# Kernel tuning notes

Measured on AMD Instinct MI355X. Metric: run time of the kernel, lower is better.

Reference implementation:

```python
import jax, jax.numpy as jnp
import numpy as np

N, FR, P, B = 8192, 128, 4194304, 64
LH1, LH2 = 128, 64

def _mlp(x, W1, b1, W2, b2, W3, b3):
    h = jnp.tanh(x @ W1 + b1)
    h = jnp.tanh(h @ W2 + b2)
    return h @ W3 + b3  # [N, 1]

def setup_inputs() -> dict:
    key = jax.random.key(0)
    ks = jax.random.split(key, 12)
    r = jax.random.normal(ks[0], (N, FR), jnp.float32)
    xyz = jax.random.uniform(ks[1], (N, 3), jnp.float32) * 60.0  # box so distances >> sigma
    p0 = jax.random.randint(ks[2], (P,), 0, N)
    off = jax.random.randint(ks[3], (P,), 1, N)  # avoid self-pairs (D2=0)
    pairs = jnp.stack([p0, (p0 + off) % N], axis=1).astype(jnp.int32)
    num_pairs = jnp.full((B,), P // B, dtype=jnp.int32)
    def lin(k, fin, fout):
        return (jax.random.normal(k, (fin, fout), jnp.float32) / np.sqrt(fin)).astype(jnp.float32)
    sW1, sW2, sW3 = lin(ks[4], FR, LH1), lin(ks[5], LH1, LH2), lin(ks[6], LH2, 1)
    eW1, eW2, eW3 = lin(ks[7], FR, LH1), lin(ks[8], LH1, LH2), lin(ks[9], LH2, 1)
    z1, z2, z3 = jnp.zeros((LH1,), jnp.float32), jnp.zeros((LH2,), jnp.float32), jnp.zeros((1,), jnp.float32)
    return dict(r=r, xyz=xyz, pairs=pairs, num_pairs=num_pairs,
                sW1=sW1, sb1=z1, sW2=sW2, sb2=z2, sW3=sW3, sb3=z3,
                eW1=eW1, eb1=z1, eW2=eW2, eb2=z2, eW3=eW3, eb3=z3)

def reference(r, xyz, pairs, num_pairs, sW1, sb1, sW2, sb2, sW3, sb3,
              eW1, eb1, eW2, eb2, eW3, eb3):
    # D2 gathered at pairs == squared distance between the two atoms of each pair
    dx = xyz[pairs[:, 1]] - xyz[pairs[:, 0]]          # [P, 3]
    D2 = jnp.sum(dx * dx, axis=1, keepdims=True)       # [P, 1]
    inv_D = D2 ** -0.5
    sigma = 4.0 + 10.0 * _mlp(r, sW1, sb1, sW2, sb2, sW3, sb3) ** 2   # [N, 1]
    epsilon = 0.1 * _mlp(r, eW1, eb1, eW2, eb2, eW3, eb3) ** 2        # [N, 1]
    sigma_mixed = jnp.sqrt(sigma[pairs[:, 0]] * sigma[pairs[:, 1]])    # [P, 1]
    epsilon_mixed = jnp.sqrt(epsilon[pairs[:, 0]] * epsilon[pairs[:, 1]])
    s = sigma_mixed * inv_D
    s6 = s ** 6
    E_pair = 4.0 * epsilon_mixed * (s6 * s6 - s6)       # [P, 1]
    seg = jnp.repeat(jnp.arange(B), num_pairs, total_repeat_length=P)
    E = jax.ops.segment_sum(E_pair, seg, num_segments=B)  # [B, 1]
    return E
```

## Files before the change

### kernel.cpp

```cpp
#include <hip/hip_runtime.h>
#include <hip/hip_fp16.h>

#define NATOM 8192
#define FR    128
#define NSEG  64
#define PB    256
#define PT    1024
#define PPT   16

typedef _Float16 v8h __attribute__((ext_vector_type(8)));
typedef _Float16 v4h __attribute__((ext_vector_type(4)));
typedef float    v4f __attribute__((ext_vector_type(4)));

__device__ __forceinline__ float fast_tanh(float x)
{
    float t = __expf(2.f * x);
    return 1.f - 2.f * __builtin_amdgcn_rcpf(t + 1.f);
}

__global__ __launch_bounds__(512) void k_prep(
    const float* __restrict__ w1s, const float* __restrict__ w1e,
    const float* __restrict__ w2s, const float* __restrict__ w2e,
    _Float16* __restrict__ planes)
{
    int i = blockIdx.x * 512 + threadIdx.x;
    if (i < 32768) {
        int c = i >> 7, k = i & 127;
        float x = (c < 128) ? w1s[k * 128 + c] : w1e[k * 128 + (c - 128)];
        _Float16 h = (_Float16)x;
        planes[i] = h;
        planes[32768 + i] = (_Float16)((x - (float)h) * 4096.f);
    } else if (i < 49152) {
        int u = i - 32768;
        int c = u >> 7, k = u & 127;
        float x = (c < 64) ? w2s[k * 64 + c] : w2e[k * 64 + (c - 64)];
        _Float16 h = (_Float16)x;
        planes[65536 + u] = h;
        planes[81920 + u] = (_Float16)((x - (float)h) * 4096.f);
    }
}

__global__ __launch_bounds__(512) void k_mm(
    const float* __restrict__ r, const float* __restrict__ xyz,
    const _Float16* __restrict__ planes,
    const float* __restrict__ b1s, const float* __restrict__ b1e,
    const float* __restrict__ b2s, const float* __restrict__ b2e,
    const float* __restrict__ w3s, const float* __restrict__ w3e,
    const float* __restrict__ b3s, const float* __restrict__ b3e,
    float4* __restrict__ atomd)
{
    extern __shared__ char ldsraw[];
    _Float16* Wh  = (_Float16*)ldsraw;
    _Float16* Wl  = Wh + 32768;
    _Float16* h1h = Wh;
    _Float16* h1l = Wh + 8192;
    _Float16* W2h = Wh + 16384;
    _Float16* W2l = Wh + 32768;
    float*    mArr = (float*)(ldsraw + 131072);

    const int tid = threadIdx.x;
    const int a0  = blockIdx.x * 32;
    const int l = tid & 63, wv = tid >> 6;
    const int row16 = l & 15, kgrp = l >> 4;
    const int at = wv & 1, cq = wv >> 1;

    {
        const uint4* ph = (const uint4*)planes;
        const uint4* pl = (const uint4*)(planes + 32768);
        uint4* dh = (uint4*)Wh; uint4* dl = (uint4*)Wl;
#pragma unroll
        for (int i = 0; i < 8; ++i) {
            int g = i * 512 + tid;
            int c = g >> 4, ch = g & 15;
            int sw = c * 16 + (ch ^ (c & 15));
            dh[sw] = ph[g]; dl[sw] = pl[g];
        }
    }

    v8h rh[4], rl[4];
    {
        const float* rb = r + (size_t)(a0 + at * 16 + row16) * FR + kgrp * 8;
#pragma unroll
        for (int ks = 0; ks < 4; ++ks) {
            float4 x0 = *(const float4*)(rb + ks * 32);
            float4 x1 = *(const float4*)(rb + ks * 32 + 4);
            float xs[8] = {x0.x, x0.y, x0.z, x0.w, x1.x, x1.y, x1.z, x1.w};
#pragma unroll
            for (int j = 0; j < 8; ++j) {
                _Float16 h = (_Float16)xs[j];
                rh[ks][j] = h;
                rl[ks][j] = (_Float16)((xs[j] - (float)h) * 4096.f);
            }
        }
    }
    __syncthreads();

    v4h hpack[4], lpack[4];
    {
#pragma unroll
        for (int ct = 0; ct < 4; ++ct) {
            int crow = cq * 64 + ct * 16 + row16;
            v4f a = {0.f, 0.f, 0.f, 0.f}, cr = {0.f, 0.f, 0.f, 0.f};
            int rbo = crow * 128, sw = crow & 15;
#pragma unroll
            for (int ks = 0; ks < 4; ++ks) {
                int off = rbo + (((ks * 4 + kgrp) ^ sw) * 8);
                v8h wh = *(const v8h*)(Wh + off);
                v8h wl = *(const v8h*)(Wl + off);
                a  = __builtin_amdgcn_mfma_f32_16x16x32_f16(wh, rh[ks], a,  0, 0, 0);
                cr = __builtin_amdgcn_mfma_f32_16x16x32_f16(wh, rl[ks], cr, 0, 0, 0);
                cr = __builtin_amdgcn_mfma_f32_16x16x32_f16(wl, rh[ks], cr, 0, 0, 0);
            }
            int colb = cq * 64 + ct * 16 + kgrp * 4;
            const float* bp = (colb < 128) ? (b1s + colb) : (b1e + (colb - 128));
            float4 bv = *(const float4*)bp;
            float bvx[4] = {bv.x, bv.y, bv.z, bv.w};
#pragma unroll
            for (int j = 0; j < 4; ++j) {
                float v = fast_tanh(a[j] + cr[j] * 2.44140625e-4f + bvx[j]);
                _Float16 h = (_Float16)v;
                hpack[ct][j] = h;
                lpack[ct][j] = (_Float16)((v - (float)h) * 4096.f);
            }
        }
    }
    __syncthreads();

    {
        int arow = at * 16 + row16;
#pragma unroll
        for (int ct = 0; ct < 4; ++ct) {
            int colb = cq * 64 + ct * 16 + kgrp * 4;
            int chs = (colb >> 3) ^ row16;
            int off = arow * 256 + chs * 8 + (colb & 7);
            *(v4h*)(h1h + off) = hpack[ct];
            *(v4h*)(h1l + off) = lpack[ct];
        }
        const uint4* ph = (const uint4*)(planes + 65536);
        const uint4* pl = (const uint4*)(planes + 81920);
        uint4* dh = (uint4*)W2h; uint4* dl = (uint4*)W2l;
#pragma unroll
        for (int i = 0; i < 4; ++i) {
            int g = i * 512 + tid;
            int c = g >> 4, ch = g & 15;
            int sw = c * 16 + (ch ^ (c & 15));
            dh[sw] = ph[g]; dl[sw] = pl[g];
        }
    }
    __syncthreads();

    {
        const int path = cq >> 1, half = cq & 1;
        const int arow = at * 16 + row16;
        v8h bh[4], bl[4];
#pragma unroll
        for (int ks = 0; ks < 4; ++ks) {
            int chunk = path * 16 + ks * 4 + kgrp;
            int off = arow * 256 + ((chunk ^ row16) * 8);
            bh[ks] = *(const v8h*)(h1h + off);
            bl[ks] = *(const v8h*)(h1l + off);
        }
        float ps = 0.f;
#pragma unroll
        for (int ct2 = 0; ct2 < 2; ++ct2) {
            int c2 = path * 64 + half * 32 + ct2 * 16 + row16;
            v4f a = {0.f, 0.f, 0.f, 0.f}, cr = {0.f, 0.f, 0.f, 0.f};
            int rbo = c2 * 128, sw = c2 & 15;
#pragma unroll
            for (int ks = 0; ks < 4; ++ks) {
                int off = rbo + (((ks * 4 + kgrp) ^ sw) * 8);
                v8h wh = *(const v8h*)(W2h + off);
                v8h wl = *(const v8h*)(W2l + off);
                a  = __builtin_amdgcn_mfma_f32_16x16x32_f16(wh, bh[ks], a,  0, 0, 0);
                cr = __builtin_amdgcn_mfma_f32_16x16x32_f16(wh, bl[ks], cr, 0, 0, 0);
                cr = __builtin_amdgcn_mfma_f32_16x16x32_f16(wl, bh[ks], cr, 0, 0, 0);
            }
            int cb = half * 32 + ct2 * 16 + kgrp * 4;
            float4 b2v = *(const float4*)((path ? b2e : b2s) + cb);
            float4 w3v = *(const float4*)((path ? w3e : w3s) + cb);
            float b2x[4] = {b2v.x, b2v.y, b2v.z, b2v.w};
            float w3x[4] = {w3v.x, w3v.y, w3v.z, w3v.w};
#pragma unroll
            for (int j = 0; j < 4; ++j) {
                float h2 = fast_tanh(a[j] + cr[j] * 2.44140625e-4f + b2x[j]);
                ps = fmaf(h2, w3x[j], ps);
            }
        }
        ps += __shfl_xor(ps, 16);
        ps += __shfl_xor(ps, 32);
        if (l < 16) mArr[cq * 32 + at * 16 + l] = ps;
    }
    __syncthreads();

    if (tid < 32) {
        int atom = a0 + tid;
        float ms = mArr[tid] + mArr[32 + tid] + b3s[0];
        float me = mArr[64 + tid] + mArr[96 + tid] + b3e[0];
        float sg = fmaf(10.f * ms, ms, 4.f);
        float p  = sg * sqrtf(sg);
        float q  = 0.31622776601683794f * fabsf(me);
        __half2 pq = __halves2half2(__float2half(p), __float2half(q));
        atomd[atom] = make_float4(xyz[3 * atom], xyz[3 * atom + 1],
                                  xyz[3 * atom + 2], __builtin_bit_cast(float, pq));
    }
}

__device__ __forceinline__ float pair_e(const float4* atomd, int ia, int ib)
{
    float4 A = atomd[ia], B = atomd[ib];
    float dx = A.x - B.x, dy = A.y - B.y, dz = A.z - B.z;
    float D2 = fmaf(dx, dx, fmaf(dy, dy, dz * dz));
    float inv = __builtin_amdgcn_rcpf(D2);
    float inv3 = inv * inv * inv;
    __half2 ha = __builtin_bit_cast(__half2, A.w);
    __half2 hb = __builtin_bit_cast(__half2, B.w);
    float pp = __low2float(ha) * __low2float(hb);
    float qq = __high2float(ha) * __high2float(hb);
    float s6 = pp * pp * inv3;
    return 4.f * qq * (s6 * s6 - s6);
}

__global__ __launch_bounds__(PT, 1) void k_pair(
    const float4* __restrict__ atomg, const int* __restrict__ pairs,
    const int* __restrict__ num_pairs,
    float* __restrict__ blocksums, int P)
{
    extern __shared__ char smem[];
    float4* atomd = (float4*)smem;
    int*    off   = (int*)(smem + NATOM * 16);
    float*  bsum  = (float*)(smem + NATOM * 16 + 68 * 4);

    const int tid = threadIdx.x;
    const int base = (blockIdx.x * PT + tid) * PPT;
    const bool fastall = __all(base + PPT <= P);

    int pr2[PPT * 2];
    if (fastall) {
        const int4* pp4 = (const int4*)(pairs + (size_t)base * 2);
#pragma unroll
        for (int i = 0; i < PPT / 2; ++i) {
            int4 v = pp4[i];
            pr2[4*i] = v.x; pr2[4*i+1] = v.y; pr2[4*i+2] = v.z; pr2[4*i+3] = v.w;
        }
    }

#pragma unroll
    for (int i = 0; i < NATOM / PT; ++i) atomd[i * PT + tid] = atomg[i * PT + tid];
    if (tid < 64) {
        int run = num_pairs[tid];
#pragma unroll
        for (int d = 1; d < 64; d <<= 1) {
            int o = __shfl_up(run, d);
            if (tid >= d) run += o;
        }
        off[tid + 1] = run;
        if (tid == 0) off[0] = 0;
        bsum[tid] = 0.f;
    }
    __syncthreads();

    if (fastall) {
        int s = 0;
#pragma unroll
        for (int st = 32; st; st >>= 1) { int ns = s + st; if (ns <= NSEG - 1 && off[ns] <= base) s = ns; }
        float acc = 0.f;
        if (base + PPT <= off[s + 1] || s == NSEG - 1) {
#pragma unroll
            for (int i = 0; i < PPT; ++i)
                acc += pair_e(atomd, pr2[2 * i], pr2[2 * i + 1]);
        } else {
            int off_next = off[s + 1];
#pragma unroll
            for (int i = 0; i < PPT; ++i) {
                int idx = base + i;
                while (s < NSEG - 1 && idx >= off_next) {
                    if (acc != 0.f) atomicAdd(&bsum[s], acc);
                    acc = 0.f; ++s; off_next = off[s + 1];
                }
                acc += pair_e(atomd, pr2[2 * i], pr2[2 * i + 1]);
            }
        }
        int s0 = __builtin_amdgcn_readfirstlane(s);
        if (__all(s == s0)) {
            float v = acc;
#pragma unroll
            for (int o = 32; o; o >>= 1) v += __shfl_xor(v, o);
            if ((tid & 63) == 0) atomicAdd(&bsum[s0], v);
        } else {
            atomicAdd(&bsum[s], acc);
        }
    } else if (base < P) {
        int s = 0;
#pragma unroll
        for (int st = 32; st; st >>= 1) { int ns = s + st; if (ns <= NSEG - 1 && off[ns] <= base) s = ns; }
        int off_next = off[s + 1];
        float acc = 0.f;
        for (int i = 0; i < PPT; ++i) {
            int idx = base + i;
            if (idx >= P) break;
            while (s < NSEG - 1 && idx >= off_next) {
                if (acc != 0.f) atomicAdd(&bsum[s], acc);
                acc = 0.f; ++s; off_next = off[s + 1];
            }
            acc += pair_e(atomd, pairs[2 * (size_t)idx], pairs[2 * (size_t)idx + 1]);
        }
        if (acc != 0.f) atomicAdd(&bsum[s], acc);
    }
    __syncthreads();
    if (tid < NSEG) blocksums[blockIdx.x * NSEG + tid] = bsum[tid];
}

__global__ __launch_bounds__(512) void k_reduce(const float* __restrict__ bs, float* __restrict__ out)
{
    __shared__ float red[8][NSEG];
    int b = threadIdx.x & 63, part = threadIdx.x >> 6;
    float s = 0.f;
    for (int j = part; j < PB; j += 8) s += bs[(size_t)j * NSEG + b];
    red[part][b] = s;
    __syncthreads();
    if (threadIdx.x < NSEG) {
        float t = 0.f;
#pragma unroll
        for (int p = 0; p < 8; ++p) t += red[p][threadIdx.x];
        out[threadIdx.x] = t;
    }
}

extern "C" void kernel_launch(void* const* d_in, const int* in_sizes, int n_in,
                              void* d_out, int out_size, void* d_ws, size_t ws_size,
                              hipStream_t stream)
{
    const float* r    = (const float*)d_in[0];
    const float* xyz  = (const float*)d_in[1];
    const int*   prs  = (const int*)d_in[2];
    const int*   np   = (const int*)d_in[3];
    const float* sW1  = (const float*)d_in[4];
    const float* sb1  = (const float*)d_in[5];
    const float* sW2  = (const float*)d_in[6];
    const float* sb2  = (const float*)d_in[7];
    const float* sW3  = (const float*)d_in[8];
    const float* sb3  = (const float*)d_in[9];
    const float* eW1  = (const float*)d_in[10];
    const float* eb1  = (const float*)d_in[11];
    const float* eW2  = (const float*)d_in[12];
    const float* eb2  = (const float*)d_in[13];
    const float* eW3  = (const float*)d_in[14];
    const float* eb3  = (const float*)d_in[15];
    float* out = (float*)d_out;
    const int P = in_sizes[2] / 2;

    _Float16* planes = (_Float16*)d_ws;
    float4*   atomd  = (float4*)((char*)d_ws + 196608);
    float*    bsums  = (float*)((char*)d_ws + 196608 + 131072);

    k_prep<<<96, 512, 0, stream>>>(sW1, eW1, sW2, eW2, planes);

    size_t smem1 = 131072 + 512;
    hipFuncSetAttribute((const void*)k_mm, hipFuncAttributeMaxDynamicSharedMemorySize, (int)smem1);
    k_mm<<<NATOM / 32, 512, smem1, stream>>>(r, xyz, planes, sb1, eb1, sb2, eb2,
                                             sW3, eW3, sb3, eb3, atomd);

    size_t smem = (size_t)NATOM * 16 + 68 * 4 + NSEG * 4;
    hipFuncSetAttribute((const void*)k_pair, hipFuncAttributeMaxDynamicSharedMemorySize, (int)smem);
    k_pair<<<PB, PT, smem, stream>>>(atomd, prs, np, bsums, P);
    k_reduce<<<1, 512, 0, stream>>>(bsums, out);
}
```

Measured before the change: 38.86 us.

## Fuse prep, MLP, pair and reduce stages into one cooperative kernel

Replaces the four separate launches with a single cooperative kernel of 256 blocks that uses grid-wide syncs between weight prep, the MLP, pair energy accumulation and the final reduction. The pair stage now runs 512 threads per block with two passes of 16 pairs each, instead of 1024 threads. The aim is to remove launch gaps and per-kernel ramp-up. The cost is grid.sync overhead, lower pair-stage concurrency per block, and occupancy limited by the 129KB LDS allocation. If the cooperative launch fails it falls back to the old four-kernel path.

```diff
diff --git a/kernel.cpp b/kernel.cpp
--- a/kernel.cpp
+++ b/kernel.cpp
@@ -1,5 +1,8 @@
 #include <hip/hip_runtime.h>
 #include <hip/hip_fp16.h>
+#include <hip/hip_cooperative_groups.h>
+
+namespace cg = cooperative_groups;
 
 #define NATOM 8192
 #define FR    128
@@ -16,6 +19,310 @@
 {
     float t = __expf(2.f * x);
     return 1.f - 2.f * __builtin_amdgcn_rcpf(t + 1.f);
+}
+
+__device__ __forceinline__ float pair_e(const float4* atomd, int ia, int ib)
+{
+    float4 A = atomd[ia], B = atomd[ib];
+    float dx = A.x - B.x, dy = A.y - B.y, dz = A.z - B.z;
+    float D2 = fmaf(dx, dx, fmaf(dy, dy, dz * dz));
+    float inv = __builtin_amdgcn_rcpf(D2);
+    float inv3 = inv * inv * inv;
+    __half2 ha = __builtin_bit_cast(__half2, A.w);
+    __half2 hb = __builtin_bit_cast(__half2, B.w);
+    float pp = __low2float(ha) * __low2float(hb);
+    float qq = __high2float(ha) * __high2float(hb);
+    float s6 = pp * pp * inv3;
+    return 4.f * qq * (s6 * s6 - s6);
+}
+
+__global__ __launch_bounds__(512) void k_all(
+    const float* __restrict__ r, const float* __restrict__ xyz,
+    const int* __restrict__ pairs, const int* __restrict__ num_pairs,
+    const float* __restrict__ w1s, const float* __restrict__ b1s,
+    const float* __restrict__ w2s, const float* __restrict__ b2s,
+    const float* __restrict__ w3s, const float* __restrict__ b3s,
+    const float* __restrict__ w1e, const float* __restrict__ b1e,
+    const float* __restrict__ w2e, const float* __restrict__ b2e,
+    const float* __restrict__ w3e, const float* __restrict__ b3e,
+    _Float16* __restrict__ planes, float4* __restrict__ atomd,
+    float* __restrict__ blocksums, float* __restrict__ out, int P)
+{
+    extern __shared__ char ldsraw[];
+    cg::grid_group grid = cg::this_grid();
+    const int tid = threadIdx.x;
+    const int bid = blockIdx.x;
+
+    {
+        int i = bid * 512 + tid;
+        if (i < 32768) {
+            int c = i >> 7, k = i & 127;
+            float x = (c < 128) ? w1s[k * 128 + c] : w1e[k * 128 + (c - 128)];
+            _Float16 h = (_Float16)x;
+            planes[i] = h;
+            planes[32768 + i] = (_Float16)((x - (float)h) * 4096.f);
+        } else if (i < 49152) {
+            int u = i - 32768;
+            int c = u >> 7, k = u & 127;
+            float x = (c < 64) ? w2s[k * 64 + c] : w2e[k * 64 + (c - 64)];
+            _Float16 h = (_Float16)x;
+            planes[65536 + u] = h;
+            planes[81920 + u] = (_Float16)((x - (float)h) * 4096.f);
+        }
+    }
+    grid.sync();
+
+    {
+        _Float16* Wh  = (_Float16*)ldsraw;
+        _Float16* Wl  = Wh + 32768;
+        _Float16* h1h = Wh;
+        _Float16* h1l = Wh + 8192;
+        _Float16* W2h = Wh + 16384;
+        _Float16* W2l = Wh + 32768;
+        float*    mArr = (float*)(ldsraw + 131072);
+
+        const int a0  = bid * 32;
+        const int l = tid & 63, wv = tid >> 6;
+        const int row16 = l & 15, kgrp = l >> 4;
+        const int at = wv & 1, cq = wv >> 1;
+
+        {
+            const uint4* ph = (const uint4*)planes;
+            const uint4* pl = (const uint4*)(planes + 32768);
+            uint4* dh = (uint4*)Wh; uint4* dl = (uint4*)Wl;
+#pragma unroll
+            for (int i = 0; i < 8; ++i) {
+                int g = i * 512 + tid;
+                int c = g >> 4, ch = g & 15;
+                int sw = c * 16 + (ch ^ (c & 15));
+                dh[sw] = ph[g]; dl[sw] = pl[g];
+            }
+        }
+
+        v8h rh[4], rl[4];
+        {
+            const float* rb = r + (size_t)(a0 + at * 16 + row16) * FR + kgrp * 8;
+#pragma unroll
+            for (int ks = 0; ks < 4; ++ks) {
+                float4 x0 = *(const float4*)(rb + ks * 32);
+                float4 x1 = *(const float4*)(rb + ks * 32 + 4);
+                float xs[8] = {x0.x, x0.y, x0.z, x0.w, x1.x, x1.y, x1.z, x1.w};
+#pragma unroll
+                for (int j = 0; j < 8; ++j) {
+                    _Float16 h = (_Float16)xs[j];
+                    rh[ks][j] = h;
+                    rl[ks][j] = (_Float16)((xs[j] - (float)h) * 4096.f);
+                }
+            }
+        }
+        __syncthreads();
+
+        v4h hpack[4], lpack[4];
+#pragma unroll
+        for (int ct = 0; ct < 4; ++ct) {
+            int crow = cq * 64 + ct * 16 + row16;
+            v4f a = {0.f, 0.f, 0.f, 0.f}, cr = {0.f, 0.f, 0.f, 0.f};
+            int rbo = crow * 128, sw = crow & 15;
+#pragma unroll
+            for (int ks = 0; ks < 4; ++ks) {
+                int off = rbo + (((ks * 4 + kgrp) ^ sw) * 8);
+                v8h wh = *(const v8h*)(Wh + off);
+                v8h wl = *(const v8h*)(Wl + off);
+                a  = __builtin_amdgcn_mfma_f32_16x16x32_f16(wh, rh[ks], a,  0, 0, 0);
+                cr = __builtin_amdgcn_mfma_f32_16x16x32_f16(wh, rl[ks], cr, 0, 0, 0);
+                cr = __builtin_amdgcn_mfma_f32_16x16x32_f16(wl, rh[ks], cr, 0, 0, 0);
+            }
+            int colb = cq * 64 + ct * 16 + kgrp * 4;
+            const float* bp = (colb < 128) ? (b1s + colb) : (b1e + (colb - 128));
+            float4 bv = *(const float4*)bp;
+            float bvx[4] = {bv.x, bv.y, bv.z, bv.w};
+#pragma unroll
+            for (int j = 0; j < 4; ++j) {
+                float v = fast_tanh(a[j] + cr[j] * 2.44140625e-4f + bvx[j]);
+                _Float16 h = (_Float16)v;
+                hpack[ct][j] = h;
+                lpack[ct][j] = (_Float16)((v - (float)h) * 4096.f);
+            }
+        }
+        __syncthreads();
+
+        {
+            int arow = at * 16 + row16;
+#pragma unroll
+            for (int ct = 0; ct < 4; ++ct) {
+                int colb = cq * 64 + ct * 16 + kgrp * 4;
+                int chs = (colb >> 3) ^ row16;
+                int off = arow * 256 + chs * 8 + (colb & 7);
+                *(v4h*)(h1h + off) = hpack[ct];
+                *(v4h*)(h1l + off) = lpack[ct];
+            }
+            const uint4* ph = (const uint4*)(planes + 65536);
+            const uint4* pl = (const uint4*)(planes + 81920);
+            uint4* dh = (uint4*)W2h; uint4* dl = (uint4*)W2l;
+#pragma unroll
+            for (int i = 0; i < 4; ++i) {
+                int g = i * 512 + tid;
+                int c = g >> 4, ch = g & 15;
+                int sw = c * 16 + (ch ^ (c & 15));
+                dh[sw] = ph[g]; dl[sw] = pl[g];
+            }
+        }
+        __syncthreads();
+
+        {
+            const int path = cq >> 1, half = cq & 1;
+            const int arow = at * 16 + row16;
+            v8h bh[4], bl[4];
+#pragma unroll
+            for (int ks = 0; ks < 4; ++ks) {
+                int chunk = path * 16 + ks * 4 + kgrp;
+                int off = arow * 256 + ((chunk ^ row16) * 8);
+                bh[ks] = *(const v8h*)(h1h + off);
+                bl[ks] = *(const v8h*)(h1l + off);
+            }
+            float ps = 0.f;
+#pragma unroll
+            for (int ct2 = 0; ct2 < 2; ++ct2) {
+                int c2 = path * 64 + half * 32 + ct2 * 16 + row16;
+                v4f a = {0.f, 0.f, 0.f, 0.f}, cr = {0.f, 0.f, 0.f, 0.f};
+                int rbo = c2 * 128, sw = c2 & 15;
+#pragma unroll
+                for (int ks = 0; ks < 4; ++ks) {
+                    int off = rbo + (((ks * 4 + kgrp) ^ sw) * 8);
+                    v8h wh = *(const v8h*)(W2h + off);
+                    v8h wl = *(const v8h*)(W2l + off);
+                    a  = __builtin_amdgcn_mfma_f32_16x16x32_f16(wh, bh[ks], a,  0, 0, 0);
+                    cr = __builtin_amdgcn_mfma_f32_16x16x32_f16(wh, bl[ks], cr, 0, 0, 0);
+                    cr = __builtin_amdgcn_mfma_f32_16x16x32_f16(wl, bh[ks], cr, 0, 0, 0);
+                }
+                int cb = half * 32 + ct2 * 16 + kgrp * 4;
+                float4 b2v = *(const float4*)((path ? b2e : b2s) + cb);
+                float4 w3v = *(const float4*)((path ? w3e : w3s) + cb);
+                float b2x[4] = {b2v.x, b2v.y, b2v.z, b2v.w};
+                float w3x[4] = {w3v.x, w3v.y, w3v.z, w3v.w};
+#pragma unroll
+                for (int j = 0; j < 4; ++j) {
+                    float h2 = fast_tanh(a[j] + cr[j] * 2.44140625e-4f + b2x[j]);
+                    ps = fmaf(h2, w3x[j], ps);
+                }
+            }
+            ps += __shfl_xor(ps, 16);
+            ps += __shfl_xor(ps, 32);
+            if (l < 16) mArr[cq * 32 + at * 16 + l] = ps;
+        }
+        __syncthreads();
+
+        if (tid < 32) {
+            int atom = a0 + tid;
+            float ms = mArr[tid] + mArr[32 + tid] + b3s[0];
+            float me = mArr[64 + tid] + mArr[96 + tid] + b3e[0];
+            float sg = fmaf(10.f * ms, ms, 4.f);
+            float p  = sg * sqrtf(sg);
+            float q  = 0.31622776601683794f * fabsf(me);
+            __half2 pq = __halves2half2(__float2half(p), __float2half(q));
+            atomd[atom] = make_float4(xyz[3 * atom], xyz[3 * atom + 1],
+                                      xyz[3 * atom + 2], __builtin_bit_cast(float, pq));
+        }
+    }
+    grid.sync();
+
+    {
+        float4* atomdL = (float4*)ldsraw;
+        int*    off    = (int*)(ldsraw + 131072);
+        float*  bsum   = (float*)(ldsraw + 131072 + 272);
+
+#pragma unroll
+        for (int i = 0; i < 16; ++i) atomdL[i * 512 + tid] = atomd[i * 512 + tid];
+        if (tid < 64) {
+            int run = num_pairs[tid];
+#pragma unroll
+            for (int d = 1; d < 64; d <<= 1) {
+                int o = __shfl_up(run, d);
+                if (tid >= d) run += o;
+            }
+            off[tid + 1] = run;
+            if (tid == 0) off[0] = 0;
+            bsum[tid] = 0.f;
+        }
+        __syncthreads();
+
+        for (int pass = 0; pass < 2; ++pass) {
+            const int base = ((bid * 512 + tid) * 2 + pass) * PPT;
+            const bool fastall = __all(base + PPT <= P);
+            if (fastall) {
+                int pr2[PPT * 2];
+                const int4* pp4 = (const int4*)(pairs + (size_t)base * 2);
+#pragma unroll
+                for (int i = 0; i < PPT / 2; ++i) {
+                    int4 v = pp4[i];
+                    pr2[4*i] = v.x; pr2[4*i+1] = v.y; pr2[4*i+2] = v.z; pr2[4*i+3] = v.w;
+                }
+                int s = 0;
+#pragma unroll
+                for (int st = 32; st; st >>= 1) { int ns = s + st; if (ns <= NSEG - 1 && off[ns] <= base) s = ns; }
+                float acc = 0.f;
+                if (base + PPT <= off[s + 1] || s == NSEG - 1) {
+#pragma unroll
+                    for (int i = 0; i < PPT; ++i)
+                        acc += pair_e(atomdL, pr2[2 * i], pr2[2 * i + 1]);
+                } else {
+                    int off_next = off[s + 1];
+#pragma unroll
+                    for (int i = 0; i < PPT; ++i) {
+                        int idx = base + i;
+                        while (s < NSEG - 1 && idx >= off_next) {
+                            if (acc != 0.f) atomicAdd(&bsum[s], acc);
+                            acc = 0.f; ++s; off_next = off[s + 1];
+                        }
+                        acc += pair_e(atomdL, pr2[2 * i], pr2[2 * i + 1]);
+                    }
+                }
+                int s0 = __builtin_amdgcn_readfirstlane(s);
+                if (__all(s == s0)) {
+                    float v = acc;
+#pragma unroll
+                    for (int o = 32; o; o >>= 1) v += __shfl_xor(v, o);
+                    if ((tid & 63) == 0) atomicAdd(&bsum[s0], v);
+                } else {
+                    atomicAdd(&bsum[s], acc);
+                }
+            } else if (base < P) {
+                int s = 0;
+#pragma unroll
+                for (int st = 32; st; st >>= 1) { int ns = s + st; if (ns <= NSEG - 1 && off[ns] <= base) s = ns; }
+                int off_next = off[s + 1];
+                float acc = 0.f;
+                for (int i = 0; i < PPT; ++i) {
+                    int idx = base + i;
+                    if (idx >= P) break;
+                    while (s < NSEG - 1 && idx >= off_next) {
+                        if (acc != 0.f) atomicAdd(&bsum[s], acc);
+                        acc = 0.f; ++s; off_next = off[s + 1];
+                    }
+                    acc += pair_e(atomdL, pairs[2 * (size_t)idx], pairs[2 * (size_t)idx + 1]);
+                }
+                if (acc != 0.f) atomicAdd(&bsum[s], acc);
+            }
+        }
+        __syncthreads();
+        if (tid < 64) blocksums[bid * 64 + tid] = bsum[tid];
+    }
+    grid.sync();
+
+    if (bid == 0) {
+        float* red = (float*)ldsraw;
+        int b = tid & 63, part = tid >> 6;
+        float s = 0.f;
+        for (int j = part; j < 256; j += 8) s += blocksums[(size_t)j * 64 + b];
+        red[part * 64 + b] = s;
+        __syncthreads();
+        if (tid < 64) {
+            float t = 0.f;
+#pragma unroll
+            for (int p = 0; p < 8; ++p) t += red[p * 64 + tid];
+            out[tid] = t;
+        }
+    }
 }
 
 __global__ __launch_bounds__(512) void k_prep(
@@ -76,7 +383,6 @@
             dh[sw] = ph[g]; dl[sw] = pl[g];
         }
     }
-
     v8h rh[4], rl[4];
     {
         const float* rb = r + (size_t)(a0 + at * 16 + row16) * FR + kgrp * 8;
@@ -96,36 +402,33 @@
     __syncthreads();
 
     v4h hpack[4], lpack[4];
-    {
-#pragma unroll
-        for (int ct = 0; ct < 4; ++ct) {
-            int crow = cq * 64 + ct * 16 + row16;
-            v4f a = {0.f, 0.f, 0.f, 0.f}, cr = {0.f, 0.f, 0.f, 0.f};
-            int rbo = crow * 128, sw = crow & 15;
-#pragma unroll
-            for (int ks = 0; ks < 4; ++ks) {
-                int off = rbo + (((ks * 4 + kgrp) ^ sw) * 8);
-                v8h wh = *(const v8h*)(Wh + off);
-                v8h wl = *(const v8h*)(Wl + off);
-                a  = __builtin_amdgcn_mfma_f32_16x16x32_f16(wh, rh[ks], a,  0, 0, 0);
-                cr = __builtin_amdgcn_mfma_f32_16x16x32_f16(wh, rl[ks], cr, 0, 0, 0);
-                cr = __builtin_amdgcn_mfma_f32_16x16x32_f16(wl, rh[ks], cr, 0, 0, 0);
-            }
-            int colb = cq * 64 + ct * 16 + kgrp * 4;
-            const float* bp = (colb < 128) ? (b1s + colb) : (b1e + (colb - 128));
-            float4 bv = *(const float4*)bp;
-            float bvx[4] = {bv.x, bv.y, bv.z, bv.w};
-#pragma unroll
-            for (int j = 0; j < 4; ++j) {
-                float v = fast_tanh(a[j] + cr[j] * 2.44140625e-4f + bvx[j]);
-                _Float16 h = (_Float16)v;
-                hpack[ct][j] = h;
-                lpack[ct][j] = (_Float16)((v - (float)h) * 4096.f);
-            }
+#pragma unroll
+    for (int ct = 0; ct < 4; ++ct) {
+        int crow = cq * 64 + ct * 16 + row16;
+        v4f a = {0.f, 0.f, 0.f, 0.f}, cr = {0.f, 0.f, 0.f, 0.f};
+        int rbo = crow * 128, sw = crow & 15;
+#pragma unroll
+        for (int ks = 0; ks < 4; ++ks) {
+            int off = rbo + (((ks * 4 + kgrp) ^ sw) * 8);
+            v8h wh = *(const v8h*)(Wh + off);
+            v8h wl = *(const v8h*)(Wl + off);
+            a  = __builtin_amdgcn_mfma_f32_16x16x32_f16(wh, rh[ks], a,  0, 0, 0);
+            cr = __builtin_amdgcn_mfma_f32_16x16x32_f16(wh, rl[ks], cr, 0, 0, 0);
+            cr = __builtin_amdgcn_mfma_f32_16x16x32_f16(wl, rh[ks], cr, 0, 0, 0);
+        }
+        int colb = cq * 64 + ct * 16 + kgrp * 4;
+        const float* bp = (colb < 128) ? (b1s + colb) : (b1e + (colb - 128));
+        float4 bv = *(const float4*)bp;
+        float bvx[4] = {bv.x, bv.y, bv.z, bv.w};
+#pragma unroll
+        for (int j = 0; j < 4; ++j) {
+            float v = fast_tanh(a[j] + cr[j] * 2.44140625e-4f + bvx[j]);
+            _Float16 h = (_Float16)v;
+            hpack[ct][j] = h;
+            lpack[ct][j] = (_Float16)((v - (float)h) * 4096.f);
         }
     }
     __syncthreads();
-
     {
         int arow = at * 16 + row16;
 #pragma unroll
@@ -148,7 +451,6 @@
         }
     }
     __syncthreads();
-
     {
         const int path = cq >> 1, half = cq & 1;
         const int arow = at * 16 + row16;
@@ -191,7 +493,6 @@
         if (l < 16) mArr[cq * 32 + at * 16 + l] = ps;
     }
     __syncthreads();
-
     if (tid < 32) {
         int atom = a0 + tid;
         float ms = mArr[tid] + mArr[32 + tid] + b3s[0];
@@ -205,21 +506,6 @@
     }
 }
 
-__device__ __forceinline__ float pair_e(const float4* atomd, int ia, int ib)
-{
-    float4 A = atomd[ia], B = atomd[ib];
-    float dx = A.x - B.x, dy = A.y - B.y, dz = A.z - B.z;
-    float D2 = fmaf(dx, dx, fmaf(dy, dy, dz * dz));
-    float inv = __builtin_amdgcn_rcpf(D2);
-    float inv3 = inv * inv * inv;
-    __half2 ha = __builtin_bit_cast(__half2, A.w);
-    __half2 hb = __builtin_bit_cast(__half2, B.w);
-    float pp = __low2float(ha) * __low2float(hb);
-    float qq = __high2float(ha) * __high2float(hb);
-    float s6 = pp * pp * inv3;
-    return 4.f * qq * (s6 * s6 - s6);
-}
-
 __global__ __launch_bounds__(PT, 1) void k_pair(
     const float4* __restrict__ atomg, const int* __restrict__ pairs,
     const int* __restrict__ num_pairs,
@@ -243,7 +529,6 @@
             pr2[4*i] = v.x; pr2[4*i+1] = v.y; pr2[4*i+2] = v.z; pr2[4*i+3] = v.w;
         }
     }
-
 #pragma unroll
     for (int i = 0; i < NATOM / PT; ++i) atomd[i * PT + tid] = atomg[i * PT + tid];
     if (tid < 64) {
@@ -347,21 +632,33 @@
     const float* eW3  = (const float*)d_in[14];
     const float* eb3  = (const float*)d_in[15];
     float* out = (float*)d_out;
-    const int P = in_sizes[2] / 2;
+    int P = in_sizes[2] / 2;
 
     _Float16* planes = (_Float16*)d_ws;
     float4*   atomd  = (float4*)((char*)d_ws + 196608);
     float*    bsums  = (float*)((char*)d_ws + 196608 + 131072);
 
-    k_prep<<<96, 512, 0, stream>>>(sW1, eW1, sW2, eW2, planes);
-
-    size_t smem1 = 131072 + 512;
-    hipFuncSetAttribute((const void*)k_mm, hipFuncAttributeMaxDynamicSharedMemorySize, (int)smem1);
-    k_mm<<<NATOM / 32, 512, smem1, stream>>>(r, xyz, planes, sb1, eb1, sb2, eb2,
-                                             sW3, eW3, sb3, eb3, atomd);
-
-    size_t smem = (size_t)NATOM * 16 + 68 * 4 + NSEG * 4;
-    hipFuncSetAttribute((const void*)k_pair, hipFuncAttributeMaxDynamicSharedMemorySize, (int)smem);
-    k_pair<<<PB, PT, smem, stream>>>(atomd, prs, np, bsums, P);
-    k_reduce<<<1, 512, 0, stream>>>(bsums, out);
-}
+    size_t smem_all = 132096;
+    hipFuncSetAttribute((const void*)k_all, hipFuncAttributeMaxDynamicSharedMemorySize, (int)smem_all);
+
+    void* args[] = { (void*)&r, (void*)&xyz, (void*)&prs, (void*)&np,
+                     (void*)&sW1, (void*)&sb1, (void*)&sW2, (void*)&sb2,
+                     (void*)&sW3, (void*)&sb3, (void*)&eW1, (void*)&eb1,
+                     (void*)&eW2, (void*)&eb2, (void*)&eW3, (void*)&eb3,
+                     (void*)&planes, (void*)&atomd, (void*)&bsums,
+                     (void*)&out, (void*)&P };
+    hipError_t e = hipLaunchCooperativeKernel((const void*)k_all, dim3(256), dim3(512),
+                                              args, (unsigned)smem_all, stream);
+    if (e != hipSuccess) {
+        (void)hipGetLastError();
+        k_prep<<<96, 512, 0, stream>>>(sW1, eW1, sW2, eW2, planes);
+        size_t smem1 = 131072 + 512;
+        hipFuncSetAttribute((const void*)k_mm, hipFuncAttributeMaxDynamicSharedMemorySize, (int)smem1);
+        k_mm<<<NATOM / 32, 512, smem1, stream>>>(r, xyz, planes, sb1, eb1, sb2, eb2,
+                                                 sW3, eW3, sb3, eb3, atomd);
+        size_t smem = (size_t)NATOM * 16 + 68 * 4 + NSEG * 4;
+        hipFuncSetAttribute((const void*)k_pair, hipFuncAttributeMaxDynamicSharedMemorySize, (int)smem);
+        k_pair<<<PB, PT, smem, stream>>>(atomd, prs, np, bsums, P);
+        k_reduce<<<1, 512, 0, stream>>>(bsums, out);
+    }
+}
```

After: 119.7 us. +208.1%, slower.
